# Kernel optimization log

Hardware: AMD Instinct MI355X
Metric: run time of the kernel (lower is better)

## Reference

```python
import jax, jax.numpy as jnp
import numpy as np

D_MODEL, D_STATE, D_CONV, EXPAND = 1024, 16, 4, 2
D_INNER = EXPAND * D_MODEL            # 2048
DT_RANK = D_MODEL // 16               # 64
B, L = 2, 4096


def setup_inputs() -> dict:
    key = jax.random.key(0)
    ks = jax.random.split(key, 8)
    s = 0.02
    u = jax.random.normal(ks[0], (B, L, D_MODEL), jnp.float32)
    in_proj_w = jax.random.normal(ks[1], (2 * D_INNER, D_MODEL), jnp.float32) * s
    conv_w = jax.random.normal(ks[2], (D_INNER, D_CONV), jnp.float32) * 0.2
    conv_b = jnp.zeros((D_INNER,), jnp.float32)
    x_proj_w = jax.random.normal(ks[3], (DT_RANK + 2 * D_STATE, D_INNER), jnp.float32) * s
    dt_proj_w = jax.random.normal(ks[4], (D_INNER, DT_RANK), jnp.float32) * (DT_RANK ** -0.5)
    # dt bias initialized so softplus(dt_bias) in [1e-3, 1e-1], as in mamba-ssm
    dt = jnp.exp(jax.random.uniform(ks[5], (D_INNER,)) * (np.log(0.1) - np.log(1e-3)) + np.log(1e-3))
    dt_bias = jnp.log(-jnp.expm1(-dt) * jnp.exp(dt))  # inverse softplus
    A_log = jnp.log(jnp.tile(jnp.arange(1, D_STATE + 1, dtype=jnp.float32), (D_INNER, 1)))
    D_in = jnp.ones((D_INNER,), jnp.float32)
    out_proj_w = jax.random.normal(ks[6], (D_MODEL, D_INNER), jnp.float32) * s
    D_skip = jnp.ones((D_MODEL,), jnp.float32)
    return dict(u=u, in_proj_w=in_proj_w, conv_w=conv_w, conv_b=conv_b,
                x_proj_w=x_proj_w, dt_proj_w=dt_proj_w, dt_bias=dt_bias,
                A_log=A_log, D_in=D_in, out_proj_w=out_proj_w, D_skip=D_skip)


def _mamba(u, in_proj_w, conv_w, conv_b, x_proj_w, dt_proj_w, dt_bias,
           A_log, D_in, out_proj_w):
    b, l, _ = u.shape
    xz = jnp.einsum('bld,ed->ble', u, in_proj_w)      # (B,L,2*Din)
    x, z = jnp.split(xz, 2, axis=-1)
    # causal depthwise conv1d over time, kernel size D_CONV
    xp = jnp.pad(x, ((0, 0), (D_CONV - 1, 0), (0, 0)))
    x = sum(xp[:, k:k + l, :] * conv_w[:, k] for k in range(D_CONV)) + conv_b
    x = jax.nn.silu(x)
    x_dbl = jnp.einsum('bld,ed->ble', x, x_proj_w)    # (B,L,dt_rank+2N)
    dt = jax.nn.softplus(x_dbl[..., :DT_RANK] @ dt_proj_w.T + dt_bias)  # (B,L,Din)
    Bm = x_dbl[..., DT_RANK:DT_RANK + D_STATE]        # (B,L,N)
    Cm = x_dbl[..., DT_RANK + D_STATE:]               # (B,L,N)
    A = -jnp.exp(A_log)                               # (Din,N)

    def step(h, inp):
        dt_t, B_t, C_t, x_t = inp                     # (B,Din),(B,N),(B,N),(B,Din)
        dA = jnp.exp(dt_t[..., None] * A)             # (B,Din,N)
        h = dA * h + (dt_t * x_t)[..., None] * B_t[:, None, :]
        y = jnp.einsum('bdn,bn->bd', h, C_t)
        return h, y

    h0 = jnp.zeros((b, D_INNER, D_STATE), u.dtype)
    xs = (dt.transpose(1, 0, 2), Bm.transpose(1, 0, 2),
          Cm.transpose(1, 0, 2), x.transpose(1, 0, 2))
    _, ys = jax.lax.scan(step, h0, xs)                # (L,B,Din)
    y = ys.transpose(1, 0, 2) + x * D_in
    y = y * jax.nn.silu(z)
    return jnp.einsum('bld,ed->ble', y, out_proj_w)   # (B,L,D_MODEL)


def reference(u, in_proj_w, conv_w, conv_b, x_proj_w, dt_proj_w, dt_bias,
              A_log, D_in, out_proj_w, D_skip):
    y = _mamba(u, in_proj_w, conv_w, conv_b, x_proj_w, dt_proj_w, dt_bias,
               A_log, D_in, out_proj_w)
    return y + D_skip[None, None, :] * u
```

## Files before the change

kernel.cpp:

```cpp
#include <hip/hip_runtime.h>

typedef unsigned short u16;
typedef unsigned int u32;
typedef __attribute__((ext_vector_type(8))) short s16x8;
typedef __attribute__((ext_vector_type(4))) float f32x4;

__device__ inline u16 f2bf(float f){
    u32 u = __float_as_uint(f);
    u32 r = (u + 0x7fffu + ((u >> 16) & 1u)) >> 16;
    return (u16)r;
}
__device__ inline float bf2f(u16 h){
    return __uint_as_float(((u32)h) << 16);
}

#define GLOAD_LDS16(g, l) __builtin_amdgcn_global_load_lds( \
    (__attribute__((address_space(1))) void*)(void*)(g),    \
    (__attribute__((address_space(3))) void*)(l), 16, 0, 0)

template<int EPI>
__global__ __launch_bounds__(256) void gemm_nt(
    const u16* __restrict__ A, const u16* __restrict__ B,
    int M, int N, int K,
    float* __restrict__ Cf, u16* __restrict__ Cb, u16* __restrict__ Cb2,
    const float* __restrict__ aux0, const float* __restrict__ aux1)
{
    constexpr int BK = 64;
    __shared__ u16 As[128 * BK];
    __shared__ u16 Bs[128 * BK];
    const int tid  = threadIdx.x;
    const int lane = tid & 63, wave = tid >> 6;
    const int wr = wave >> 1, wc = wave & 1;
    const int bm = blockIdx.x, bn = blockIdx.y;
    const int l16 = lane & 15, lg = lane >> 4;

    const u16* Ab = A + (size_t)bm * 128 * K;
    const u16* Bb = B + (size_t)bn * 128 * K;

    f32x4 acc[4][4] = {};

    for (int kt = 0; kt < K; kt += BK) {
        #pragma unroll
        for (int p = 0; p < 4; p++) {
            int flat = (p * 256 + tid) * 8;
            int r = flat >> 6, c = flat & 63;
            GLOAD_LDS16(Ab + (size_t)r * K + kt + c, As + flat);
        }
        #pragma unroll
        for (int p = 0; p < 4; p++) {
            int flat = (p * 256 + tid) * 8;
            int r = flat >> 6, c = flat & 63;
            GLOAD_LDS16(Bb + (size_t)r * K + kt + c, Bs + flat);
        }
        asm volatile("s_waitcnt vmcnt(0)" ::: "memory");
        __syncthreads();
        #pragma unroll
        for (int kk = 0; kk < 2; kk++) {
            s16x8 a[4], b[4];
            #pragma unroll
            for (int m = 0; m < 4; m++)
                a[m] = *(const s16x8*)&As[(wr * 64 + m * 16 + l16) * BK + kk * 32 + lg * 8];
            #pragma unroll
            for (int n = 0; n < 4; n++)
                b[n] = *(const s16x8*)&Bs[(wc * 64 + n * 16 + l16) * BK + kk * 32 + lg * 8];
            #pragma unroll
            for (int m = 0; m < 4; m++)
                #pragma unroll
                for (int n = 0; n < 4; n++)
                    acc[m][n] = __builtin_amdgcn_mfma_f32_16x16x32_bf16(a[m], b[n], acc[m][n], 0, 0, 0);
        }
        __syncthreads();
    }

    const int row0 = bm * 128 + wr * 64 + lg * 4;
    const int col0 = bn * 128 + wc * 64 + l16;
    #pragma unroll
    for (int m = 0; m < 4; m++) {
        #pragma unroll
        for (int n = 0; n < 4; n++) {
            const int col = col0 + n * 16;
            #pragma unroll
            for (int r = 0; r < 4; r++) {
                const int row = row0 + m * 16 + r;
                float v = acc[m][n][r];
                if (EPI == 0) {
                    if (col < 2048) Cb[(size_t)row * 2048 + col] = f2bf(v);
                    else            Cb2[(size_t)row * 2048 + (col - 2048)] = f2bf(v);
                } else if (EPI == 2) {
                    float t2 = v + aux0[col];
                    float sp = (t2 > 15.f) ? t2 : __logf(1.f + __expf(t2));
                    Cb[(size_t)row * N + col] = f2bf(sp);
                } else {
                    float o = v + aux0[col] * aux1[(size_t)row * N + col];
                    Cf[(size_t)row * N + col] = o;
                }
            }
        }
    }
}

__global__ __launch_bounds__(256) void gemm_xproj_sk(
    const u16* __restrict__ A, const u16* __restrict__ B,
    float* __restrict__ part)
{
    constexpr int BK = 64, K = 2048;
    __shared__ u16 As[128 * BK];
    __shared__ u16 Bs[128 * BK];
    const int tid  = threadIdx.x;
    const int lane = tid & 63, wave = tid >> 6;
    const int wr = wave >> 1, wc = wave & 1;
    const int bm = blockIdx.x, sk = blockIdx.y;
    const int l16 = lane & 15, lg = lane >> 4;

    const u16* Ab = A + (size_t)bm * 128 * K;
    const u16* Bb = B;
    const int kt0 = sk * 256;

    f32x4 acc[4][4] = {};

    for (int kt = kt0; kt < kt0 + 256; kt += BK) {
        #pragma unroll
        for (int p = 0; p < 4; p++) {
            int flat = (p * 256 + tid) * 8;
            int r = flat >> 6, c = flat & 63;
            GLOAD_LDS16(Ab + (size_t)r * K + kt + c, As + flat);
        }
        #pragma unroll
        for (int p = 0; p < 4; p++) {
            int flat = (p * 256 + tid) * 8;
            int r = flat >> 6, c = flat & 63;
            GLOAD_LDS16(Bb + (size_t)r * K + kt + c, Bs + flat);
        }
        asm volatile("s_waitcnt vmcnt(0)" ::: "memory");
        __syncthreads();
        #pragma unroll
        for (int kk = 0; kk < 2; kk++) {
            s16x8 a[4], b[4];
            #pragma unroll
            for (int m = 0; m < 4; m++)
                a[m] = *(const s16x8*)&As[(wr * 64 + m * 16 + l16) * BK + kk * 32 + lg * 8];
            #pragma unroll
            for (int n = 0; n < 4; n++)
                b[n] = *(const s16x8*)&Bs[(wc * 64 + n * 16 + l16) * BK + kk * 32 + lg * 8];
            #pragma unroll
            for (int m = 0; m < 4; m++)
                #pragma unroll
                for (int n = 0; n < 4; n++)
                    acc[m][n] = __builtin_amdgcn_mfma_f32_16x16x32_bf16(a[m], b[n], acc[m][n], 0, 0, 0);
        }
        __syncthreads();
    }

    float* pb = part + (size_t)sk * 8192 * 128;
    const int row0 = bm * 128 + wr * 64 + lg * 4;
    const int col0 = wc * 64 + l16;
    #pragma unroll
    for (int m = 0; m < 4; m++)
        #pragma unroll
        for (int n = 0; n < 4; n++)
            #pragma unroll
            for (int r = 0; r < 4; r++)
                pb[(size_t)(row0 + m * 16 + r) * 128 + col0 + n * 16] = acc[m][n][r];
}

__global__ __launch_bounds__(256) void combine_xproj(
    const float* __restrict__ part, u16* __restrict__ dtin,
    float* __restrict__ xBC)
{
    const int gid = blockIdx.x * 256 + threadIdx.x;
    const int row = gid >> 7, col = gid & 127;
    float s = 0.f;
    #pragma unroll
    for (int sk = 0; sk < 8; sk++) s += part[(size_t)sk * 8192 * 128 + gid];
    if (col < 64)      dtin[(size_t)row * 64 + col] = f2bf(s);
    else if (col < 96) xBC[(size_t)row * 32 + (col - 64)] = s;
}

__global__ void cvt_f32_bf16(const float* __restrict__ in, u16* __restrict__ out, int n)
{
    int i = (blockIdx.x * 256 + threadIdx.x) * 4;
    if (i < n) {
        f32x4 v = *(const f32x4*)(in + i);
        ushort4 o;
        o.x = f2bf(v[0]); o.y = f2bf(v[1]); o.z = f2bf(v[2]); o.w = f2bf(v[3]);
        *(ushort4*)(out + i) = o;
    }
}

__global__ void cvt_pad_xproj(const float* __restrict__ in, u16* __restrict__ out)
{
    int i = blockIdx.x * 256 + threadIdx.x;
    int row = i >> 11, col = i & 2047;
    float v = (row < 96) ? in[row * 2048 + col] : 0.f;
    out[i] = f2bf(v);
}

__global__ __launch_bounds__(256) void conv_silu(
    const u16* __restrict__ xzx, const float* __restrict__ cw,
    const float* __restrict__ cb, u16* __restrict__ xc)
{
    const int tid = threadIdx.x;
    const int dl = tid & 63, tg = tid >> 6;
    const int d = blockIdx.y * 64 + dl;
    const int t0 = blockIdx.x * 64 + tg * 16;
    const int b = blockIdx.z;
    const float c0 = cw[d * 4 + 0], c1 = cw[d * 4 + 1];
    const float c2 = cw[d * 4 + 2], c3 = cw[d * 4 + 3];
    const float bias = cb[d];
    const u16* xp = xzx + (size_t)(b * 4096) * 2048 + d;
    u16* op = xc + (size_t)(b * 4096) * 2048 + d;
    float w0 = (t0 >= 3) ? bf2f(xp[(size_t)(t0 - 3) * 2048]) : 0.f;
    float w1 = (t0 >= 2) ? bf2f(xp[(size_t)(t0 - 2) * 2048]) : 0.f;
    float w2 = (t0 >= 1) ? bf2f(xp[(size_t)(t0 - 1) * 2048]) : 0.f;
    #pragma unroll
    for (int k = 0; k < 16; k++) {
        int t = t0 + k;
        float cur = bf2f(xp[(size_t)t * 2048]);
        float s = bias + w0 * c0 + w1 * c1 + w2 * c2 + cur * c3;
        float v = s * __fdividef(1.f, 1.f + __expf(-s));
        op[(size_t)t * 2048] = f2bf(v);
        w0 = w1; w1 = w2; w2 = cur;
    }
}

__global__ __launch_bounds__(256) void scan_p1(
    const u16* __restrict__ dtb, const u16* __restrict__ xc,
    const float* __restrict__ xBC, const float* __restrict__ A_log,
    u16* __restrict__ Aagg, u16* __restrict__ Bagg)
{
    __shared__ float Bsh[64][16];
    const int tid = threadIdx.x;
    const int d = blockIdx.x * 256 + tid;
    const int c = blockIdx.y, b = blockIdx.z;

    {
        int ti = tid >> 2, p = tid & 3;
        f32x4 bv = *(const f32x4*)(xBC + ((size_t)(b * 4096 + c * 64 + ti)) * 32 + p * 4);
        *(f32x4*)&Bsh[ti][p * 4] = bv;
    }
    __syncthreads();

    float Adn[16];
    #pragma unroll
    for (int q = 0; q < 4; q++) {
        f32x4 al = *(const f32x4*)(A_log + (size_t)d * 16 + q * 4);
        #pragma unroll
        for (int j = 0; j < 4; j++) Adn[q * 4 + j] = -__expf(al[j]);
    }

    const size_t base = (size_t)(b * 4096 + c * 64) * 2048 + d;
    const u16* dtp = dtb + base;
    const u16* xp  = xc  + base;

    float h[16];
    #pragma unroll
    for (int n = 0; n < 16; n++) h[n] = 0.f;
    float sumdt = 0.f;

    float dtv = bf2f(dtp[0]), xv = bf2f(xp[0]);
    for (int t = 0; t < 64; t++) {
        float ndt = 0.f, nx = 0.f;
        if (t < 63) { ndt = bf2f(dtp[(size_t)(t + 1) * 2048]); nx = bf2f(xp[(size_t)(t + 1) * 2048]); }
        float dtx = dtv * xv;
        sumdt += dtv;
        f32x4 B0 = *(const f32x4*)&Bsh[t][0];
        f32x4 B1 = *(const f32x4*)&Bsh[t][4];
        f32x4 B2 = *(const f32x4*)&Bsh[t][8];
        f32x4 B3 = *(const f32x4*)&Bsh[t][12];
        #pragma unroll
        for (int n = 0; n < 16; n++) {
            float Bv = (n < 4) ? B0[n] : (n < 8) ? B1[n - 4] : (n < 12) ? B2[n - 8] : B3[n - 12];
            float a = __expf(Adn[n] * dtv);
            h[n] = fmaf(a, h[n], dtx * Bv);
        }
        dtv = ndt; xv = nx;
    }

    const size_t abase = ((size_t)(b * 2048 + d) * 16) * 64 + c;
    #pragma unroll
    for (int n = 0; n < 16; n++) {
        Aagg[abase + (size_t)n * 64] = f2bf(__expf(Adn[n] * sumdt));
        Bagg[abase + (size_t)n * 64] = f2bf(h[n]);
    }
}

__global__ __launch_bounds__(256) void scan_p2(
    const u16* __restrict__ Aagg, u16* __restrict__ BaggH0)
{
    const int gid = blockIdx.x * 256 + threadIdx.x;
    const size_t base = (size_t)gid * 64;
    s16x8 Ar[8], Br[8];
    #pragma unroll
    for (int i = 0; i < 8; i++) {
        Ar[i] = *(const s16x8*)(Aagg + base + i * 8);
        Br[i] = *(const s16x8*)(BaggH0 + base + i * 8);
    }
    s16x8 Hr[8];
    float h = 0.f;
    #pragma unroll
    for (int i = 0; i < 8; i++) {
        #pragma unroll
        for (int j = 0; j < 8; j++) {
            float ac = bf2f((u16)Ar[i][j]);
            float bc = bf2f((u16)Br[i][j]);
            Hr[i][j] = (short)f2bf(h);
            h = fmaf(ac, h, bc);
        }
    }
    #pragma unroll
    for (int i = 0; i < 8; i++)
        *(s16x8*)(BaggH0 + base + i * 8) = Hr[i];
}

__global__ __launch_bounds__(256) void scan_p3(
    const u16* __restrict__ dtb, const u16* __restrict__ xc,
    const float* __restrict__ xBC, const float* __restrict__ A_log,
    const u16* __restrict__ H0, const u16* __restrict__ xzz,
    const float* __restrict__ D_in, u16* __restrict__ yy)
{
    __shared__ float BCs[64][32];
    const int tid = threadIdx.x;
    const int d = blockIdx.x * 256 + tid;
    const int c = blockIdx.y, b = blockIdx.z;

    {
        int ti = tid >> 2, p = tid & 3;
        const float* src = xBC + ((size_t)(b * 4096 + c * 64 + ti)) * 32 + p * 8;
        f32x4 v0 = *(const f32x4*)src;
        f32x4 v1 = *(const f32x4*)(src + 4);
        *(f32x4*)&BCs[ti][p * 8] = v0;
        *(f32x4*)&BCs[ti][p * 8 + 4] = v1;
    }
    __syncthreads();

    float Adn[16];
    #pragma unroll
    for (int q = 0; q < 4; q++) {
        f32x4 al = *(const f32x4*)(A_log + (size_t)d * 16 + q * 4);
        #pragma unroll
        for (int j = 0; j < 4; j++) Adn[q * 4 + j] = -__expf(al[j]);
    }
    const float Dd = D_in[d];

    float h[16];
    const size_t hbase = ((size_t)(b * 2048 + d) * 16) * 64 + c;
    #pragma unroll
    for (int n = 0; n < 16; n++) h[n] = bf2f(H0[hbase + (size_t)n * 64]);

    const size_t base = (size_t)(b * 4096 + c * 64) * 2048 + d;
    const u16* dtp = dtb + base;
    const u16* xp  = xc  + base;
    const u16* zp  = xzz + base;
    u16* yp = yy + base;

    float dtv = bf2f(dtp[0]), xv = bf2f(xp[0]), zv = bf2f(zp[0]);
    for (int t = 0; t < 64; t++) {
        float ndt = 0.f, nx = 0.f, nz = 0.f;
        if (t < 63) {
            ndt = bf2f(dtp[(size_t)(t + 1) * 2048]);
            nx  = bf2f(xp[(size_t)(t + 1) * 2048]);
            nz  = bf2f(zp[(size_t)(t + 1) * 2048]);
        }
        float dtx = dtv * xv;
        f32x4 B0 = *(const f32x4*)&BCs[t][0];
        f32x4 B1 = *(const f32x4*)&BCs[t][4];
        f32x4 B2 = *(const f32x4*)&BCs[t][8];
        f32x4 B3 = *(const f32x4*)&BCs[t][12];
        f32x4 C0 = *(const f32x4*)&BCs[t][16];
        f32x4 C1 = *(const f32x4*)&BCs[t][20];
        f32x4 C2 = *(const f32x4*)&BCs[t][24];
        f32x4 C3 = *(const f32x4*)&BCs[t][28];
        float y = 0.f;
        #pragma unroll
        for (int n = 0; n < 16; n++) {
            float Bv = (n < 4) ? B0[n] : (n < 8) ? B1[n - 4] : (n < 12) ? B2[n - 8] : B3[n - 12];
            float Cv = (n < 4) ? C0[n] : (n < 8) ? C1[n - 4] : (n < 12) ? C2[n - 8] : C3[n - 12];
            float a = __expf(Adn[n] * dtv);
            h[n] = fmaf(a, h[n], dtx * Bv);
            y = fmaf(h[n], Cv, y);
        }
        float sz = zv * __fdividef(1.f, 1.f + __expf(-zv));
        float val = fmaf(xv, Dd, y) * sz;
        yp[(size_t)t * 2048] = f2bf(val);
        dtv = ndt; xv = nx; zv = nz;
    }
}

extern "C" void kernel_launch(void* const* d_in, const int* in_sizes, int n_in,
                              void* d_out, int out_size, void* d_ws, size_t ws_size,
                              hipStream_t stream)
{
    const float* u       = (const float*)d_in[0];
    const float* Wi      = (const float*)d_in[1];
    const float* conv_w  = (const float*)d_in[2];
    const float* conv_b  = (const float*)d_in[3];
    const float* Wx      = (const float*)d_in[4];
    const float* Wdt     = (const float*)d_in[5];
    const float* dt_bias = (const float*)d_in[6];
    const float* A_log   = (const float*)d_in[7];
    const float* D_in_   = (const float*)d_in[8];
    const float* Wo      = (const float*)d_in[9];
    const float* D_skip  = (const float*)d_in[10];
    float* out = (float*)d_out;
    (void)in_sizes; (void)n_in; (void)out_size;

    const size_t MB = 1u << 20;
    char* ws = (char*)d_ws;
    u16*   xzx    = (u16*)(ws + 0);
    float* xpart  = (float*)(ws + 0);
    u16*   Aagg   = (u16*)(ws + 0);
    u16*   BaggH0 = (u16*)(ws + 8 * MB);
    u16*   xzz    = (u16*)(ws + 32 * MB);
    u16*   xc     = (u16*)(ws + 64 * MB);
    u16*   u_bf   = (u16*)(ws + 96 * MB);
    u16*   Wi_bf  = (u16*)(ws + 112 * MB);
    u16*   dtb    = (u16*)(ws + 96 * MB);
    u16*   Wx_bf  = (u16*)(ws + 128 * MB);
    u16*   Wdt_bf = (u16*)(ws + 128 * MB + 512 * 1024);
    u16*   yybuf  = (u16*)(ws + 128 * MB);
    float* xBC    = (float*)(ws + 160 * MB);
    u16*   dtin   = (u16*)(ws + 161 * MB);
    u16*   Wo_bf  = (u16*)(ws + 162 * MB);
    const size_t NEED = 166 * MB;
    if (ws_size < NEED) return;

    cvt_f32_bf16<<<8192, 256, 0, stream>>>(u, u_bf, 8388608);
    cvt_f32_bf16<<<4096, 256, 0, stream>>>(Wi, Wi_bf, 4194304);
    cvt_f32_bf16<<<2048, 256, 0, stream>>>(Wo, Wo_bf, 2097152);
    cvt_f32_bf16<<<128, 256, 0, stream>>>(Wdt, Wdt_bf, 131072);
    cvt_pad_xproj<<<1024, 256, 0, stream>>>(Wx, Wx_bf);

    gemm_nt<0><<<dim3(64, 32), 256, 0, stream>>>(u_bf, Wi_bf, 8192, 4096, 1024,
                                                 nullptr, xzx, xzz, nullptr, nullptr);
    conv_silu<<<dim3(64, 32, 2), 256, 0, stream>>>(xzx, conv_w, conv_b, xc);

    gemm_xproj_sk<<<dim3(64, 8), 256, 0, stream>>>(xc, Wx_bf, xpart);
    combine_xproj<<<4096, 256, 0, stream>>>(xpart, dtin, xBC);

    gemm_nt<2><<<dim3(64, 16), 256, 0, stream>>>(dtin, Wdt_bf, 8192, 2048, 64,
                                                 nullptr, dtb, nullptr, dt_bias, nullptr);

    scan_p1<<<dim3(8, 64, 2), 256, 0, stream>>>(dtb, xc, xBC, A_log, Aagg, BaggH0);
    scan_p2<<<256, 256, 0, stream>>>(Aagg, BaggH0);
    scan_p3<<<dim3(8, 64, 2), 256, 0, stream>>>(dtb, xc, xBC, A_log, BaggH0, xzz,
                                                D_in_, yybuf);

    gemm_nt<3><<<dim3(64, 8), 256, 0, stream>>>(yybuf, Wo_bf, 8192, 1024, 2048,
                                                out, nullptr, nullptr, D_skip, u);
}
```

Baseline: 409.1 us.

## Double-buffer GEMM LDS tiles, swizzle workgroups, fuse conversions, vectorize conv

```diff
diff --git a/kernel.cpp b/kernel.cpp
--- a/kernel.cpp
+++ b/kernel.cpp
@@ -21,56 +21,73 @@
 template<int EPI>
 __global__ __launch_bounds__(256) void gemm_nt(
     const u16* __restrict__ A, const u16* __restrict__ B,
-    int M, int N, int K,
+    int M, int N, int K, int nbn,
     float* __restrict__ Cf, u16* __restrict__ Cb, u16* __restrict__ Cb2,
     const float* __restrict__ aux0, const float* __restrict__ aux1)
 {
     constexpr int BK = 64;
-    __shared__ u16 As[128 * BK];
-    __shared__ u16 Bs[128 * BK];
+    __shared__ u16 As[2][128 * BK];
+    __shared__ u16 Bs[2][128 * BK];
     const int tid  = threadIdx.x;
     const int lane = tid & 63, wave = tid >> 6;
     const int wr = wave >> 1, wc = wave & 1;
-    const int bm = blockIdx.x, bn = blockIdx.y;
     const int l16 = lane & 15, lg = lane >> 4;
+
+    int wgid = blockIdx.x;
+    int nwg  = gridDim.x;
+    int swz  = wgid;
+    if ((nwg & 7) == 0) { int cpx = nwg >> 3; swz = (wgid & 7) * cpx + (wgid >> 3); }
+    const int bm = swz / nbn, bn = swz % nbn;
 
     const u16* Ab = A + (size_t)bm * 128 * K;
     const u16* Bb = B + (size_t)bn * 128 * K;
 
     f32x4 acc[4][4] = {};
 
-    for (int kt = 0; kt < K; kt += BK) {
+    auto stage = [&](int buf, int kt) {
         #pragma unroll
         for (int p = 0; p < 4; p++) {
             int flat = (p * 256 + tid) * 8;
             int r = flat >> 6, c = flat & 63;
-            GLOAD_LDS16(Ab + (size_t)r * K + kt + c, As + flat);
+            GLOAD_LDS16(Ab + (size_t)r * K + kt + c, &As[buf][flat]);
         }
         #pragma unroll
         for (int p = 0; p < 4; p++) {
             int flat = (p * 256 + tid) * 8;
             int r = flat >> 6, c = flat & 63;
-            GLOAD_LDS16(Bb + (size_t)r * K + kt + c, Bs + flat);
-        }
-        asm volatile("s_waitcnt vmcnt(0)" ::: "memory");
-        __syncthreads();
+            GLOAD_LDS16(Bb + (size_t)r * K + kt + c, &Bs[buf][flat]);
+        }
+    };
+    auto compute = [&](int buf) {
         #pragma unroll
         for (int kk = 0; kk < 2; kk++) {
             s16x8 a[4], b[4];
             #pragma unroll
             for (int m = 0; m < 4; m++)
-                a[m] = *(const s16x8*)&As[(wr * 64 + m * 16 + l16) * BK + kk * 32 + lg * 8];
+                a[m] = *(const s16x8*)&As[buf][(wr * 64 + m * 16 + l16) * BK + kk * 32 + lg * 8];
             #pragma unroll
             for (int n = 0; n < 4; n++)
-                b[n] = *(const s16x8*)&Bs[(wc * 64 + n * 16 + l16) * BK + kk * 32 + lg * 8];
+                b[n] = *(const s16x8*)&Bs[buf][(wc * 64 + n * 16 + l16) * BK + kk * 32 + lg * 8];
             #pragma unroll
             for (int m = 0; m < 4; m++)
                 #pragma unroll
                 for (int n = 0; n < 4; n++)
                     acc[m][n] = __builtin_amdgcn_mfma_f32_16x16x32_bf16(a[m], b[n], acc[m][n], 0, 0, 0);
         }
+    };
+
+    stage(0, 0);
+    asm volatile("s_waitcnt vmcnt(0)" ::: "memory");
+    __syncthreads();
+    int cur = 0;
+    for (int kt = BK; kt < K; kt += BK) {
+        stage(cur ^ 1, kt);
+        compute(cur);
+        asm volatile("s_waitcnt vmcnt(0)" ::: "memory");
         __syncthreads();
-    }
+        cur ^= 1;
+    }
+    compute(cur);
 
     const int row0 = bm * 128 + wr * 64 + lg * 4;
     const int col0 = bn * 128 + wc * 64 + l16;
@@ -104,8 +121,8 @@
     float* __restrict__ part)
 {
     constexpr int BK = 64, K = 2048;
-    __shared__ u16 As[128 * BK];
-    __shared__ u16 Bs[128 * BK];
+    __shared__ u16 As[2][128 * BK];
+    __shared__ u16 Bs[2][128 * BK];
     const int tid  = threadIdx.x;
     const int lane = tid & 63, wave = tid >> 6;
     const int wr = wave >> 1, wc = wave & 1;
@@ -118,38 +135,50 @@
 
     f32x4 acc[4][4] = {};
 
-    for (int kt = kt0; kt < kt0 + 256; kt += BK) {
+    auto stage = [&](int buf, int kt) {
         #pragma unroll
         for (int p = 0; p < 4; p++) {
             int flat = (p * 256 + tid) * 8;
             int r = flat >> 6, c = flat & 63;
-            GLOAD_LDS16(Ab + (size_t)r * K + kt + c, As + flat);
+            GLOAD_LDS16(Ab + (size_t)r * K + kt + c, &As[buf][flat]);
         }
         #pragma unroll
         for (int p = 0; p < 4; p++) {
             int flat = (p * 256 + tid) * 8;
             int r = flat >> 6, c = flat & 63;
-            GLOAD_LDS16(Bb + (size_t)r * K + kt + c, Bs + flat);
-        }
-        asm volatile("s_waitcnt vmcnt(0)" ::: "memory");
-        __syncthreads();
+            GLOAD_LDS16(Bb + (size_t)r * K + kt + c, &Bs[buf][flat]);
+        }
+    };
+    auto compute = [&](int buf) {
         #pragma unroll
         for (int kk = 0; kk < 2; kk++) {
             s16x8 a[4], b[4];
             #pragma unroll
             for (int m = 0; m < 4; m++)
-                a[m] = *(const s16x8*)&As[(wr * 64 + m * 16 + l16) * BK + kk * 32 + lg * 8];
+                a[m] = *(const s16x8*)&As[buf][(wr * 64 + m * 16 + l16) * BK + kk * 32 + lg * 8];
             #pragma unroll
             for (int n = 0; n < 4; n++)
-                b[n] = *(const s16x8*)&Bs[(wc * 64 + n * 16 + l16) * BK + kk * 32 + lg * 8];
+                b[n] = *(const s16x8*)&Bs[buf][(wc * 64 + n * 16 + l16) * BK + kk * 32 + lg * 8];
             #pragma unroll
             for (int m = 0; m < 4; m++)
                 #pragma unroll
                 for (int n = 0; n < 4; n++)
                     acc[m][n] = __builtin_amdgcn_mfma_f32_16x16x32_bf16(a[m], b[n], acc[m][n], 0, 0, 0);
         }
+    };
+
+    stage(0, kt0);
+    asm volatile("s_waitcnt vmcnt(0)" ::: "memory");
+    __syncthreads();
+    int cur = 0;
+    for (int kt = kt0 + BK; kt < kt0 + 256; kt += BK) {
+        stage(cur ^ 1, kt);
+        compute(cur);
+        asm volatile("s_waitcnt vmcnt(0)" ::: "memory");
         __syncthreads();
-    }
+        cur ^= 1;
+    }
+    compute(cur);
 
     float* pb = part + (size_t)sk * 8192 * 128;
     const int row0 = bm * 128 + wr * 64 + lg * 4;
@@ -176,23 +205,32 @@
     else if (col < 96) xBC[(size_t)row * 32 + (col - 64)] = s;
 }
 
-__global__ void cvt_f32_bf16(const float* __restrict__ in, u16* __restrict__ out, int n)
-{
-    int i = (blockIdx.x * 256 + threadIdx.x) * 4;
-    if (i < n) {
-        f32x4 v = *(const f32x4*)(in + i);
-        ushort4 o;
-        o.x = f2bf(v[0]); o.y = f2bf(v[1]); o.z = f2bf(v[2]); o.w = f2bf(v[3]);
-        *(ushort4*)(out + i) = o;
-    }
-}
-
-__global__ void cvt_pad_xproj(const float* __restrict__ in, u16* __restrict__ out)
-{
-    int i = blockIdx.x * 256 + threadIdx.x;
-    int row = i >> 11, col = i & 2047;
-    float v = (row < 96) ? in[row * 2048 + col] : 0.f;
-    out[i] = f2bf(v);
+__global__ __launch_bounds__(256) void cvt_all(
+    const float* __restrict__ u, const float* __restrict__ Wi,
+    const float* __restrict__ Wo, const float* __restrict__ Wdt,
+    const float* __restrict__ Wx,
+    u16* __restrict__ u_bf, u16* __restrict__ Wi_bf, u16* __restrict__ Wo_bf,
+    u16* __restrict__ Wdt_bf, u16* __restrict__ Wx_bf)
+{
+    size_t i = ((size_t)blockIdx.x * 256 + threadIdx.x) * 4;
+    const size_t E0 = 8388608, E1 = E0 + 4194304, E2 = E1 + 2097152, E3 = E2 + 131072;
+    f32x4 v;
+    u16* dst;
+    size_t off;
+    if (i < E0)      { off = i;      v = *(const f32x4*)(u + off);   dst = u_bf + off; }
+    else if (i < E1) { off = i - E0; v = *(const f32x4*)(Wi + off);  dst = Wi_bf + off; }
+    else if (i < E2) { off = i - E1; v = *(const f32x4*)(Wo + off);  dst = Wo_bf + off; }
+    else if (i < E3) { off = i - E2; v = *(const f32x4*)(Wdt + off); dst = Wdt_bf + off; }
+    else {
+        off = i - E3;
+        size_t row = off >> 11;
+        if (row < 96) v = *(const f32x4*)(Wx + off);
+        else          v = (f32x4){0.f, 0.f, 0.f, 0.f};
+        dst = Wx_bf + off;
+    }
+    ushort4 o;
+    o.x = f2bf(v[0]); o.y = f2bf(v[1]); o.z = f2bf(v[2]); o.w = f2bf(v[3]);
+    *(ushort4*)dst = o;
 }
 
 __global__ __launch_bounds__(256) void conv_silu(
@@ -200,26 +238,45 @@
     const float* __restrict__ cb, u16* __restrict__ xc)
 {
     const int tid = threadIdx.x;
-    const int dl = tid & 63, tg = tid >> 6;
-    const int d = blockIdx.y * 64 + dl;
-    const int t0 = blockIdx.x * 64 + tg * 16;
-    const int b = blockIdx.z;
-    const float c0 = cw[d * 4 + 0], c1 = cw[d * 4 + 1];
-    const float c2 = cw[d * 4 + 2], c3 = cw[d * 4 + 3];
-    const float bias = cb[d];
-    const u16* xp = xzx + (size_t)(b * 4096) * 2048 + d;
-    u16* op = xc + (size_t)(b * 4096) * 2048 + d;
-    float w0 = (t0 >= 3) ? bf2f(xp[(size_t)(t0 - 3) * 2048]) : 0.f;
-    float w1 = (t0 >= 2) ? bf2f(xp[(size_t)(t0 - 2) * 2048]) : 0.f;
-    float w2 = (t0 >= 1) ? bf2f(xp[(size_t)(t0 - 1) * 2048]) : 0.f;
+    const int d0 = tid * 8;
+    const int t0 = blockIdx.x * 16;
+    const int b  = blockIdx.y;
+    float W0[8], W1[8], W2[8], W3[8], BI[8];
+    #pragma unroll
+    for (int j = 0; j < 8; j++) {
+        f32x4 w = *(const f32x4*)(cw + (size_t)(d0 + j) * 4);
+        W0[j] = w[0]; W1[j] = w[1]; W2[j] = w[2]; W3[j] = w[3];
+        BI[j] = cb[d0 + j];
+    }
+    const u16* xp = xzx + (size_t)(b * 4096) * 2048 + d0;
+    u16* op = xc + (size_t)(b * 4096) * 2048 + d0;
+
+    float x0[8], x1[8], x2[8];
+    #pragma unroll
+    for (int j = 0; j < 8; j++) { x0[j] = 0.f; x1[j] = 0.f; x2[j] = 0.f; }
+    if (t0 >= 3) {
+        s16x8 v0 = *(const s16x8*)(xp + (size_t)(t0 - 3) * 2048);
+        s16x8 v1 = *(const s16x8*)(xp + (size_t)(t0 - 2) * 2048);
+        s16x8 v2 = *(const s16x8*)(xp + (size_t)(t0 - 1) * 2048);
+        #pragma unroll
+        for (int j = 0; j < 8; j++) {
+            x0[j] = bf2f((u16)v0[j]); x1[j] = bf2f((u16)v1[j]); x2[j] = bf2f((u16)v2[j]);
+        }
+    }
     #pragma unroll
     for (int k = 0; k < 16; k++) {
         int t = t0 + k;
-        float cur = bf2f(xp[(size_t)t * 2048]);
-        float s = bias + w0 * c0 + w1 * c1 + w2 * c2 + cur * c3;
-        float v = s * __fdividef(1.f, 1.f + __expf(-s));
-        op[(size_t)t * 2048] = f2bf(v);
-        w0 = w1; w1 = w2; w2 = cur;
+        s16x8 cv = *(const s16x8*)(xp + (size_t)t * 2048);
+        s16x8 o;
+        #pragma unroll
+        for (int j = 0; j < 8; j++) {
+            float c = bf2f((u16)cv[j]);
+            float s = BI[j] + W0[j] * x0[j] + W1[j] * x1[j] + W2[j] * x2[j] + W3[j] * c;
+            float v = s * __fdividef(1.f, 1.f + __expf(-s));
+            o[j] = (short)f2bf(v);
+            x0[j] = x1[j]; x1[j] = x2[j]; x2[j] = c;
+        }
+        *(s16x8*)(op + (size_t)t * 2048) = o;
     }
 }
 
@@ -424,27 +481,24 @@
     const size_t NEED = 166 * MB;
     if (ws_size < NEED) return;
 
-    cvt_f32_bf16<<<8192, 256, 0, stream>>>(u, u_bf, 8388608);
-    cvt_f32_bf16<<<4096, 256, 0, stream>>>(Wi, Wi_bf, 4194304);
-    cvt_f32_bf16<<<2048, 256, 0, stream>>>(Wo, Wo_bf, 2097152);
-    cvt_f32_bf16<<<128, 256, 0, stream>>>(Wdt, Wdt_bf, 131072);
-    cvt_pad_xproj<<<1024, 256, 0, stream>>>(Wx, Wx_bf);
-
-    gemm_nt<0><<<dim3(64, 32), 256, 0, stream>>>(u_bf, Wi_bf, 8192, 4096, 1024,
-                                                 nullptr, xzx, xzz, nullptr, nullptr);
-    conv_silu<<<dim3(64, 32, 2), 256, 0, stream>>>(xzx, conv_w, conv_b, xc);
+    cvt_all<<<14720, 256, 0, stream>>>(u, Wi, Wo, Wdt, Wx,
+                                       u_bf, Wi_bf, Wo_bf, Wdt_bf, Wx_bf);
+
+    gemm_nt<0><<<2048, 256, 0, stream>>>(u_bf, Wi_bf, 8192, 4096, 1024, 32,
+                                         nullptr, xzx, xzz, nullptr, nullptr);
+    conv_silu<<<dim3(256, 2), 256, 0, stream>>>(xzx, conv_w, conv_b, xc);
 
     gemm_xproj_sk<<<dim3(64, 8), 256, 0, stream>>>(xc, Wx_bf, xpart);
     combine_xproj<<<4096, 256, 0, stream>>>(xpart, dtin, xBC);
 
-    gemm_nt<2><<<dim3(64, 16), 256, 0, stream>>>(dtin, Wdt_bf, 8192, 2048, 64,
-                                                 nullptr, dtb, nullptr, dt_bias, nullptr);
+    gemm_nt<2><<<1024, 256, 0, stream>>>(dtin, Wdt_bf, 8192, 2048, 64, 16,
+                                         nullptr, dtb, nullptr, dt_bias, nullptr);
 
     scan_p1<<<dim3(8, 64, 2), 256, 0, stream>>>(dtb, xc, xBC, A_log, Aagg, BaggH0);
     scan_p2<<<256, 256, 0, stream>>>(Aagg, BaggH0);
     scan_p3<<<dim3(8, 64, 2), 256, 0, stream>>>(dtb, xc, xBC, A_log, BaggH0, xzz,
                                                 D_in_, yybuf);
 
-    gemm_nt<3><<<dim3(64, 8), 256, 0, stream>>>(yybuf, Wo_bf, 8192, 1024, 2048,
-                                                out, nullptr, nullptr, D_skip, u);
-}
+    gemm_nt<3><<<512, 256, 0, stream>>>(yybuf, Wo_bf, 8192, 1024, 2048, 8,
+                                        out, nullptr, nullptr, D_skip, u);
+}
```

Result: slower. 436.6 us (+6.7%).
